# Kernel optimization log

Hardware: AMD Instinct MI355X
Metric: run time of the kernel (lower is better)

## Reference

```python
import jax, jax.numpy as jnp
import numpy as np
import math

B, L, D, H = 2, 2048, 1024, 16
HS = D // H  # head size 64


def setup_inputs() -> dict:
    key = jax.random.key(0)
    ks = jax.random.split(key, 4)
    s = 1.0 / math.sqrt(D)
    return {
        "x": jax.random.normal(ks[0], (B, L, D), dtype=jnp.float32),
        "mask": jnp.zeros((B, 1, L, L), dtype=jnp.float32),
        "Wq": jax.random.normal(ks[1], (D, D), dtype=jnp.float32) * s,
        "bq": jnp.zeros((D,), dtype=jnp.float32),
        "Wk": jax.random.normal(ks[2], (D, D), dtype=jnp.float32) * s,
        "bk": jnp.zeros((D,), dtype=jnp.float32),
        "Wv": jax.random.normal(ks[3], (D, D), dtype=jnp.float32) * s,
        "bv": jnp.zeros((D,), dtype=jnp.float32),
    }


def reference(x, mask, Wq, bq, Wk, bk, Wv, bv):
    # projections: torch Linear is x @ W.T + b
    q = (x @ Wq.T + bq).reshape(B, L, H, HS).transpose(0, 2, 1, 3)  # [B,H,L,hs]
    k = (x @ Wk.T + bk).reshape(B, L, H, HS).transpose(0, 2, 1, 3)
    v = (x @ Wv.T + bv).reshape(B, L, H, HS).transpose(0, 2, 1, 3)
    scores = jnp.einsum("bhqd,bhkd->bhqk", q, k) / math.sqrt(HS) + mask
    attn = jax.nn.softmax(scores, axis=-1)  # dropout p=0.0 -> identity
    out = jnp.einsum("bhqk,bhkd->bhqd", attn, v)
    return out.transpose(0, 2, 1, 3).reshape(B, L, D)
```

## Files before the change

kernel.cpp:

```cpp
#include <hip/hip_runtime.h>
#include <cstdint>

#define SEQ 2048
#define DMODEL 1024
#define NHEAD 16
#define HEADSZ 64

typedef __attribute__((ext_vector_type(4))) float f32x4;
typedef __attribute__((ext_vector_type(8))) short short8;
typedef __attribute__((ext_vector_type(4))) unsigned short u16x4;

#define AS1 __attribute__((address_space(1)))
#define AS3 __attribute__((address_space(3)))

__device__ __forceinline__ void gload_lds16(const void* g, void* l) {
  __builtin_amdgcn_global_load_lds((const AS1 void*)g, (AS3 void*)l, 16, 0, 0);
}

__device__ __forceinline__ unsigned short f2bf(float f) {
  unsigned u = __float_as_uint(f);
  u += 0x7fffu + ((u >> 16) & 1u);
  return (unsigned short)(u >> 16);
}

__global__ __launch_bounds__(256) void convert_kernel(
    const float* __restrict__ x, const float* __restrict__ wq,
    const float* __restrict__ wk, const float* __restrict__ wv,
    unsigned short* __restrict__ xb, unsigned short* __restrict__ wb) {
  const long i = ((long)blockIdx.x * 256 + threadIdx.x) * 4;
  const float* src;
  unsigned short* dst;
  if (i < (1L << 22)) {
    src = x + i; dst = xb + i;
  } else {
    const long j = i - (1L << 22);
    dst = wb + j;
    if (j < (1L << 20))        src = wq + j;
    else if (j < (2L << 20))   src = wk + (j - (1L << 20));
    else                       src = wv + (j - (2L << 20));
  }
  f32x4 v = *(const f32x4*)src;
  u16x4 o;
  o.x = f2bf(v.x); o.y = f2bf(v.y); o.z = f2bf(v.z); o.w = f2bf(v.w);
  *(u16x4*)dst = o;
}

__global__ __launch_bounds__(256) void qkv_gemm(
    const unsigned short* __restrict__ xb, const unsigned short* __restrict__ wb,
    const float* __restrict__ bq, const float* __restrict__ bk,
    const float* __restrict__ bv,
    unsigned short* __restrict__ qo, unsigned short* __restrict__ ko,
    unsigned short* __restrict__ vto) {
  __shared__ __attribute__((aligned(16))) unsigned short Sh[2][128 * 64];
  unsigned short* As = &Sh[0][0];
  unsigned short* Bs = &Sh[1][0];

  const int bid = blockIdx.x;
  const int swz = (bid & 7) * 96 + (bid >> 3);
  const int tm = swz / 24, tn = swz % 24;
  const int m0 = tm * 128, n0 = tn * 128;
  const int tsel = n0 >> 10;
  const int t = threadIdx.x;
  const int lane = t & 63, wid = t >> 6;
  const int wr = wid >> 1, wc = wid & 1;
  const int r16 = lane & 15, g4 = lane >> 4;

  f32x4 acc[4][4] = {};

  const unsigned short* ga0 = xb + (long)(m0 + (t >> 3)) * 1024 + (t & 7) * 8;
  const unsigned short* gb0 = wb + (long)(n0 + (t >> 3)) * 1024 + (t & 7) * 8;
  char* lA = (char*)As + wid * 1024;
  char* lB = (char*)Bs + wid * 1024;

  for (int ks = 0; ks < 16; ++ks) {
    const unsigned short* ga = ga0 + ks * 64;
    const unsigned short* gb = gb0 + ks * 64;
#pragma unroll
    for (int r = 0; r < 4; ++r) {
      gload_lds16(ga + r * 32 * 1024, lA + r * 4096);
      gload_lds16(gb + r * 32 * 1024, lB + r * 4096);
    }
    __syncthreads();
#pragma unroll
    for (int kk = 0; kk < 2; ++kk) {
      short8 af[4], bf[4];
#pragma unroll
      for (int mi = 0; mi < 4; ++mi)
        af[mi] = *(const short8*)((const char*)As +
                 (wr * 64 + mi * 16 + r16) * 128 + kk * 64 + g4 * 16);
#pragma unroll
      for (int ni = 0; ni < 4; ++ni)
        bf[ni] = *(const short8*)((const char*)Bs +
                 (wc * 64 + ni * 16 + r16) * 128 + kk * 64 + g4 * 16);
      if (tsel < 2) {
#pragma unroll
        for (int mi = 0; mi < 4; ++mi)
#pragma unroll
          for (int ni = 0; ni < 4; ++ni)
            acc[mi][ni] = __builtin_amdgcn_mfma_f32_16x16x32_bf16(
                bf[ni], af[mi], acc[mi][ni], 0, 0, 0);
      } else {
#pragma unroll
        for (int mi = 0; mi < 4; ++mi)
#pragma unroll
          for (int ni = 0; ni < 4; ++ni)
            acc[mi][ni] = __builtin_amdgcn_mfma_f32_16x16x32_bf16(
                af[mi], bf[ni], acc[mi][ni], 0, 0, 0);
      }
    }
    __syncthreads();
  }

  const int bb = m0 >> 11;
  const int lbase = m0 & 2047;
  const int h0n = n0 & 1023;
  unsigned short* T = As;

  if (tsel < 2) {
    const float* bias = tsel == 0 ? bq : bk;
    unsigned short* dst01 = tsel == 0 ? qo : ko;
#pragma unroll
    for (int ni = 0; ni < 4; ++ni) {
      const int nlb = wc * 64 + ni * 16 + g4 * 4;
      const f32x4 b4 = *(const f32x4*)(bias + h0n + nlb);
#pragma unroll
      for (int mi = 0; mi < 4; ++mi) {
        const int ml = wr * 64 + mi * 16 + r16;
        u16x4 pk;
#pragma unroll
        for (int i = 0; i < 4; ++i) pk[i] = f2bf(acc[mi][ni][i] + b4[i]);
        int byteoff = ml * 256 + nlb * 2;
        byteoff ^= (ml & 7) << 4;
        *(u16x4*)((char*)T + byteoff) = pk;
      }
    }
    __syncthreads();
#pragma unroll
    for (int p = 0; p < 8; ++p) {
      const int ml = p * 16 + (t >> 4);
      int byteoff = ml * 256 + ((t & 15) << 4);
      byteoff ^= (ml & 7) << 4;
      short8 row = *(const short8*)((const char*)T + byteoff);
      const int nd = h0n + (t & 15) * 8;
      const int h = nd >> 6, hs = nd & 63;
      *(short8*)(dst01 + ((long)(bb * NHEAD + h) * SEQ + lbase + ml) * 64 + hs) = row;
    }
  } else {
#pragma unroll
    for (int ni = 0; ni < 4; ++ni) {
      const int nl = wc * 64 + ni * 16 + r16;
      const float bval = bv[h0n + nl];
#pragma unroll
      for (int mi = 0; mi < 4; ++mi) {
        const int mlb = wr * 64 + mi * 16 + g4 * 4;
        u16x4 pk;
#pragma unroll
        for (int i = 0; i < 4; ++i) pk[i] = f2bf(acc[mi][ni][i] + bval);
        int byteoff = nl * 256 + mlb * 2;
        byteoff ^= (nl & 7) << 4;
        *(u16x4*)((char*)T + byteoff) = pk;
      }
    }
    __syncthreads();
#pragma unroll
    for (int p = 0; p < 8; ++p) {
      const int nl = p * 16 + (t >> 4);
      int byteoff = nl * 256 + ((t & 15) << 4);
      byteoff ^= (nl & 7) << 4;
      short8 row = *(const short8*)((const char*)T + byteoff);
      const int nd = h0n + nl;
      const int h = nd >> 6, hs = nd & 63;
      *(short8*)(vto + ((((long)(bb * NHEAD + h)) << 6) + hs) * SEQ + lbase +
                 (t & 15) * 8) = row;
    }
  }
}

__global__ __launch_bounds__(256, 4) void attn_kernel(
    const unsigned short* __restrict__ qb, const unsigned short* __restrict__ kb,
    const unsigned short* __restrict__ vtb, const float* __restrict__ mask,
    float* __restrict__ out) {
  __shared__ __attribute__((aligned(16))) unsigned short Qs[64 * 64];
  __shared__ __attribute__((aligned(16))) unsigned short Ks[2][64 * 64];
  __shared__ __attribute__((aligned(16))) unsigned short Vs[2][64 * 64];

  const int bid = blockIdx.x;
  const int swz = (bid & 7) * 128 + (bid >> 3);
  const int h = swz & 15, rest = swz >> 4;
  const int qt = rest & 31, b = rest >> 5;
  const int bh = b * NHEAD + h;

  const unsigned short* qg = qb + (long)bh * SEQ * 64 + qt * 64 * 64;
  const unsigned short* kg = kb + (long)bh * SEQ * 64;
  const unsigned short* vg = vtb + (long)bh * 64 * SEQ;
  const float* mg = mask + (long)b * SEQ * SEQ + (long)(qt * 64) * SEQ;

  const int t = threadIdx.x;
  const int lane = t & 63, w = t >> 6;
  const int r16 = lane & 15, g4 = lane >> 4;
  const int rowa = t >> 3;
  const int csel = ((t & 7) ^ (rowa & 7)) * 8;
  const int swzr = (r16 & 7);

  auto stageKV = [&](int ktile, int buf) {
#pragma unroll
    for (int r = 0; r < 2; ++r) {
      gload_lds16(kg + (long)(ktile * 64 + r * 32 + rowa) * 64 + csel,
                  (char*)Ks + buf * 8192 + r * 4096 + w * 1024);
      gload_lds16(vg + (long)(r * 32 + rowa) * SEQ + ktile * 64 + csel,
                  (char*)Vs + buf * 8192 + r * 4096 + w * 1024);
    }
  };

#pragma unroll
  for (int r = 0; r < 2; ++r)
    gload_lds16(qg + (r * 256 + t) * 8, (char*)Qs + r * 4096 + w * 1024);
  stageKV(0, 0);
  __syncthreads();

  short8 qf[2];
#pragma unroll
  for (int kk = 0; kk < 2; ++kk)
    qf[kk] = *(const short8*)((const char*)Qs +
              (w * 16 + r16) * 128 + kk * 64 + g4 * 16);
  char* Pw = (char*)Qs + w * 2048;

  float m_st[4], l_st[4];
  f32x4 o_acc[4] = {};
#pragma unroll
  for (int i = 0; i < 4; ++i) { m_st[i] = -1e30f; l_st[i] = 0.f; }

  int cur = 0;
  for (int kt = 0; kt < 32; ++kt) {
    if (kt < 31) stageKV(kt + 1, cur ^ 1);

    const char* Kb = (const char*)Ks + cur * 8192;
    const char* Vb = (const char*)Vs + cur * 8192;

    float mv[4][4];
#pragma unroll
    for (int nf = 0; nf < 4; ++nf)
#pragma unroll
      for (int i = 0; i < 4; ++i)
        mv[nf][i] = mg[(long)(w * 16 + g4 * 4 + i) * SEQ +
                       kt * 64 + nf * 16 + r16];

    f32x4 s[4];
#pragma unroll
    for (int nf = 0; nf < 4; ++nf) {
      f32x4 z = {};
#pragma unroll
      for (int kk = 0; kk < 2; ++kk) {
        short8 kf = *(const short8*)(Kb + (nf * 16 + r16) * 128 +
                     (((kk * 4 + g4) ^ swzr) << 4));
        z = __builtin_amdgcn_mfma_f32_16x16x32_bf16(qf[kk], kf, z, 0, 0, 0);
      }
      s[nf] = z;
    }
#pragma unroll
    for (int nf = 0; nf < 4; ++nf)
#pragma unroll
      for (int i = 0; i < 4; ++i)
        s[nf][i] = s[nf][i] * 0.125f + mv[nf][i];

    float pm[4];
#pragma unroll
    for (int i = 0; i < 4; ++i)
      pm[i] = fmaxf(fmaxf(s[0][i], s[1][i]), fmaxf(s[2][i], s[3][i]));
#pragma unroll
    for (int x = 1; x <= 8; x <<= 1)
#pragma unroll
      for (int i = 0; i < 4; ++i)
        pm[i] = fmaxf(pm[i], __shfl_xor(pm[i], x, 64));
    float alpha[4], rs[4];
#pragma unroll
    for (int i = 0; i < 4; ++i) {
      const float mn = fmaxf(m_st[i], pm[i]);
      alpha[i] = __expf(m_st[i] - mn);
      m_st[i] = mn;
      rs[i] = 0.f;
    }
#pragma unroll
    for (int nf = 0; nf < 4; ++nf)
#pragma unroll
      for (int i = 0; i < 4; ++i) {
        const float p = __expf(s[nf][i] - m_st[i]);
        rs[i] += p;
        const int q = g4 * 4 + i;
        int byteoff = q * 128 + (nf * 16 + r16) * 2;
        byteoff ^= (q & 7) << 4;
        *(unsigned short*)(Pw + byteoff) = f2bf(p);
      }
#pragma unroll
    for (int x = 1; x <= 8; x <<= 1)
#pragma unroll
      for (int i = 0; i < 4; ++i)
        rs[i] += __shfl_xor(rs[i], x, 64);
#pragma unroll
    for (int i = 0; i < 4; ++i)
      l_st[i] = l_st[i] * alpha[i] + rs[i];
#pragma unroll
    for (int nd = 0; nd < 4; ++nd)
#pragma unroll
      for (int i = 0; i < 4; ++i)
        o_acc[nd][i] *= alpha[i];

    asm volatile("s_waitcnt lgkmcnt(0)" ::: "memory");
    short8 pa[2];
#pragma unroll
    for (int kk = 0; kk < 2; ++kk)
      pa[kk] = *(const short8*)(Pw + r16 * 128 + (((kk * 4 + g4) ^ swzr) << 4));
#pragma unroll
    for (int nd = 0; nd < 4; ++nd) {
      f32x4 z = o_acc[nd];
#pragma unroll
      for (int kk = 0; kk < 2; ++kk) {
        short8 vf = *(const short8*)(Vb + (nd * 16 + r16) * 128 +
                     (((kk * 4 + g4) ^ swzr) << 4));
        z = __builtin_amdgcn_mfma_f32_16x16x32_bf16(pa[kk], vf, z, 0, 0, 0);
      }
      o_acc[nd] = z;
    }

    __syncthreads();
    cur ^= 1;
  }

  float* ob = out + (long)b * SEQ * DMODEL + (long)(qt * 64) * DMODEL + h * 64;
#pragma unroll
  for (int nd = 0; nd < 4; ++nd)
#pragma unroll
    for (int i = 0; i < 4; ++i) {
      const int qrow = w * 16 + g4 * 4 + i;
      ob[(long)qrow * DMODEL + nd * 16 + r16] = o_acc[nd][i] / l_st[i];
    }
}

extern "C" void kernel_launch(void* const* d_in, const int* in_sizes, int n_in,
                              void* d_out, int out_size, void* d_ws, size_t ws_size,
                              hipStream_t stream) {
  const float* x    = (const float*)d_in[0];
  const float* mask = (const float*)d_in[1];
  const float* Wq   = (const float*)d_in[2];
  const float* bq   = (const float*)d_in[3];
  const float* Wk   = (const float*)d_in[4];
  const float* bk   = (const float*)d_in[5];
  const float* Wv   = (const float*)d_in[6];
  const float* bv   = (const float*)d_in[7];
  float* out = (float*)d_out;

  char* ws = (char*)d_ws;
  unsigned short* xb  = (unsigned short*)(ws);
  unsigned short* wb  = (unsigned short*)(ws + (8L << 20));
  unsigned short* qo  = (unsigned short*)(ws + (14L << 20));
  unsigned short* ko  = (unsigned short*)(ws + (22L << 20));
  unsigned short* vto = (unsigned short*)(ws + (30L << 20));

  convert_kernel<<<7168, 256, 0, stream>>>(x, Wq, Wk, Wv, xb, wb);
  qkv_gemm<<<768, 256, 0, stream>>>(xb, wb, bq, bk, bv, qo, ko, vto);
  attn_kernel<<<1024, 256, 0, stream>>>(qo, ko, vto, mask, out);
}
```

Before: 268.3 us.

## Restructure attention to 32x32 MFMA with 128-row query tiles and register P

```diff
diff --git a/kernel.cpp b/kernel.cpp
--- a/kernel.cpp
+++ b/kernel.cpp
@@ -7,8 +7,10 @@
 #define HEADSZ 64
 
 typedef __attribute__((ext_vector_type(4))) float f32x4;
+typedef __attribute__((ext_vector_type(16))) float f32x16;
 typedef __attribute__((ext_vector_type(8))) short short8;
 typedef __attribute__((ext_vector_type(4))) unsigned short u16x4;
+typedef __attribute__((ext_vector_type(4))) unsigned int u32x4;
 
 #define AS1 __attribute__((address_space(1)))
 #define AS3 __attribute__((address_space(3)))
@@ -21,6 +23,10 @@
   unsigned u = __float_as_uint(f);
   u += 0x7fffu + ((u >> 16) & 1u);
   return (unsigned short)(u >> 16);
+}
+
+__device__ __forceinline__ unsigned pack2bf(float lo, float hi) {
+  return (unsigned)f2bf(lo) | ((unsigned)f2bf(hi) << 16);
 }
 
 __global__ __launch_bounds__(256) void convert_kernel(
@@ -176,59 +182,54 @@
   }
 }
 
-__global__ __launch_bounds__(256, 4) void attn_kernel(
+__global__ __launch_bounds__(256, 2) void attn_kernel(
     const unsigned short* __restrict__ qb, const unsigned short* __restrict__ kb,
     const unsigned short* __restrict__ vtb, const float* __restrict__ mask,
     float* __restrict__ out) {
-  __shared__ __attribute__((aligned(16))) unsigned short Qs[64 * 64];
-  __shared__ __attribute__((aligned(16))) unsigned short Ks[2][64 * 64];
-  __shared__ __attribute__((aligned(16))) unsigned short Vs[2][64 * 64];
+  __shared__ __attribute__((aligned(16))) char lds[34816];
+  unsigned short* Ks = (unsigned short*)lds;
+  unsigned short* Vs = (unsigned short*)(lds + 16384);
 
   const int bid = blockIdx.x;
-  const int swz = (bid & 7) * 128 + (bid >> 3);
-  const int h = swz & 15, rest = swz >> 4;
-  const int qt = rest & 31, b = rest >> 5;
+  const int swz = (bid & 7) * 64 + (bid >> 3);
+  const int h = swz & 15, grp = swz >> 4;
+  const int qt = grp & 15, b = grp >> 4;
   const int bh = b * NHEAD + h;
 
-  const unsigned short* qg = qb + (long)bh * SEQ * 64 + qt * 64 * 64;
+  const int t = threadIdx.x;
+  const int lane = t & 63, w = t >> 6;
+  const int lq = lane & 31;
+  const int hi = lane >> 5;
+
+  const unsigned short* qg = qb + (long)bh * SEQ * 64;
   const unsigned short* kg = kb + (long)bh * SEQ * 64;
   const unsigned short* vg = vtb + (long)bh * 64 * SEQ;
-  const float* mg = mask + (long)b * SEQ * SEQ + (long)(qt * 64) * SEQ;
-
-  const int t = threadIdx.x;
-  const int lane = t & 63, w = t >> 6;
-  const int r16 = lane & 15, g4 = lane >> 4;
-  const int rowa = t >> 3;
-  const int csel = ((t & 7) ^ (rowa & 7)) * 8;
-  const int swzr = (r16 & 7);
-
-  auto stageKV = [&](int ktile, int buf) {
+  const int q0 = qt * 128 + w * 32;
+  const float* mrow = mask + (long)b * SEQ * SEQ + (long)(q0 + lq) * SEQ;
+
+  auto stageKV = [&](int kt, int buf) {
 #pragma unroll
     for (int r = 0; r < 2; ++r) {
-      gload_lds16(kg + (long)(ktile * 64 + r * 32 + rowa) * 64 + csel,
-                  (char*)Ks + buf * 8192 + r * 4096 + w * 1024);
-      gload_lds16(vg + (long)(r * 32 + rowa) * SEQ + ktile * 64 + csel,
-                  (char*)Vs + buf * 8192 + r * 4096 + w * 1024);
+      const int row = w * 16 + r * 8 + (lane >> 3);
+      const int gsw = ((lane & 7) ^ (row & 7)) * 8;
+      gload_lds16(kg + (long)(kt * 64 + row) * 64 + gsw,
+                  (char*)Ks + buf * 8192 + w * 2048 + r * 1024);
+      gload_lds16(vg + (long)row * SEQ + kt * 64 + gsw,
+                  (char*)Vs + buf * 8192 + w * 2048 + r * 1024);
     }
   };
 
-#pragma unroll
-  for (int r = 0; r < 2; ++r)
-    gload_lds16(qg + (r * 256 + t) * 8, (char*)Qs + r * 4096 + w * 1024);
   stageKV(0, 0);
+
+  short8 qf[4];
+#pragma unroll
+  for (int kk = 0; kk < 4; ++kk)
+    qf[kk] = *(const short8*)(qg + (long)(q0 + lq) * 64 + hi * 8 + kk * 16);
+
+  f32x16 oa0 = {}, oa1 = {};
+  float m_st = -1e30f, l_st = 0.f;
+
   __syncthreads();
-
-  short8 qf[2];
-#pragma unroll
-  for (int kk = 0; kk < 2; ++kk)
-    qf[kk] = *(const short8*)((const char*)Qs +
-              (w * 16 + r16) * 128 + kk * 64 + g4 * 16);
-  char* Pw = (char*)Qs + w * 2048;
-
-  float m_st[4], l_st[4];
-  f32x4 o_acc[4] = {};
-#pragma unroll
-  for (int i = 0; i < 4; ++i) { m_st[i] = -1e30f; l_st[i] = 0.f; }
 
   int cur = 0;
   for (int kt = 0; kt < 32; ++kt) {
@@ -237,103 +238,101 @@
     const char* Kb = (const char*)Ks + cur * 8192;
     const char* Vb = (const char*)Vs + cur * 8192;
 
-    float mv[4][4];
-#pragma unroll
-    for (int nf = 0; nf < 4; ++nf)
-#pragma unroll
-      for (int i = 0; i < 4; ++i)
-        mv[nf][i] = mg[(long)(w * 16 + g4 * 4 + i) * SEQ +
-                       kt * 64 + nf * 16 + r16];
-
-    f32x4 s[4];
-#pragma unroll
-    for (int nf = 0; nf < 4; ++nf) {
-      f32x4 z = {};
-#pragma unroll
-      for (int kk = 0; kk < 2; ++kk) {
-        short8 kf = *(const short8*)(Kb + (nf * 16 + r16) * 128 +
-                     (((kk * 4 + g4) ^ swzr) << 4));
-        z = __builtin_amdgcn_mfma_f32_16x16x32_bf16(qf[kk], kf, z, 0, 0, 0);
-      }
-      s[nf] = z;
-    }
-#pragma unroll
-    for (int nf = 0; nf < 4; ++nf)
-#pragma unroll
-      for (int i = 0; i < 4; ++i)
-        s[nf][i] = s[nf][i] * 0.125f + mv[nf][i];
-
-    float pm[4];
-#pragma unroll
-    for (int i = 0; i < 4; ++i)
-      pm[i] = fmaxf(fmaxf(s[0][i], s[1][i]), fmaxf(s[2][i], s[3][i]));
-#pragma unroll
-    for (int x = 1; x <= 8; x <<= 1)
-#pragma unroll
-      for (int i = 0; i < 4; ++i)
-        pm[i] = fmaxf(pm[i], __shfl_xor(pm[i], x, 64));
-    float alpha[4], rs[4];
-#pragma unroll
-    for (int i = 0; i < 4; ++i) {
-      const float mn = fmaxf(m_st[i], pm[i]);
-      alpha[i] = __expf(m_st[i] - mn);
-      m_st[i] = mn;
-      rs[i] = 0.f;
-    }
-#pragma unroll
-    for (int nf = 0; nf < 4; ++nf)
-#pragma unroll
-      for (int i = 0; i < 4; ++i) {
-        const float p = __expf(s[nf][i] - m_st[i]);
-        rs[i] += p;
-        const int q = g4 * 4 + i;
-        int byteoff = q * 128 + (nf * 16 + r16) * 2;
-        byteoff ^= (q & 7) << 4;
-        *(unsigned short*)(Pw + byteoff) = f2bf(p);
-      }
-#pragma unroll
-    for (int x = 1; x <= 8; x <<= 1)
-#pragma unroll
-      for (int i = 0; i < 4; ++i)
-        rs[i] += __shfl_xor(rs[i], x, 64);
-#pragma unroll
-    for (int i = 0; i < 4; ++i)
-      l_st[i] = l_st[i] * alpha[i] + rs[i];
-#pragma unroll
-    for (int nd = 0; nd < 4; ++nd)
-#pragma unroll
-      for (int i = 0; i < 4; ++i)
-        o_acc[nd][i] *= alpha[i];
-
-    asm volatile("s_waitcnt lgkmcnt(0)" ::: "memory");
-    short8 pa[2];
-#pragma unroll
-    for (int kk = 0; kk < 2; ++kk)
-      pa[kk] = *(const short8*)(Pw + r16 * 128 + (((kk * 4 + g4) ^ swzr) << 4));
-#pragma unroll
-    for (int nd = 0; nd < 4; ++nd) {
-      f32x4 z = o_acc[nd];
-#pragma unroll
-      for (int kk = 0; kk < 2; ++kk) {
-        short8 vf = *(const short8*)(Vb + (nd * 16 + r16) * 128 +
-                     (((kk * 4 + g4) ^ swzr) << 4));
-        z = __builtin_amdgcn_mfma_f32_16x16x32_bf16(pa[kk], vf, z, 0, 0, 0);
-      }
-      o_acc[nd] = z;
+    f32x4 mv[2][4];
+#pragma unroll
+    for (int k2 = 0; k2 < 2; ++k2)
+#pragma unroll
+      for (int g = 0; g < 4; ++g)
+        mv[k2][g] = *(const f32x4*)(mrow + kt * 64 + k2 * 32 + g * 8 + hi * 4);
+
+    f32x16 sa0 = {}, sa1 = {};
+#pragma unroll
+    for (int kk = 0; kk < 4; ++kk) {
+      const int r0 = lq;
+      short8 kf0 = *(const short8*)(Kb + r0 * 128 + (((hi + 2 * kk) ^ (r0 & 7)) << 4));
+      sa0 = __builtin_amdgcn_mfma_f32_32x32x16_bf16(kf0, qf[kk], sa0, 0, 0, 0);
+      const int r1 = 32 + lq;
+      short8 kf1 = *(const short8*)(Kb + r1 * 128 + (((hi + 2 * kk) ^ (r1 & 7)) << 4));
+      sa1 = __builtin_amdgcn_mfma_f32_32x32x16_bf16(kf1, qf[kk], sa1, 0, 0, 0);
+    }
+
+    float s[32];
+#pragma unroll
+    for (int r = 0; r < 16; ++r)
+      s[r] = sa0[r] * 0.125f + mv[0][r >> 2][r & 3];
+#pragma unroll
+    for (int r = 0; r < 16; ++r)
+      s[16 + r] = sa1[r] * 0.125f + mv[1][r >> 2][r & 3];
+
+    float pm = s[0];
+#pragma unroll
+    for (int r = 1; r < 32; ++r) pm = fmaxf(pm, s[r]);
+    pm = fmaxf(pm, __shfl_xor(pm, 32, 64));
+    const float mn = fmaxf(m_st, pm);
+    const float alpha = __expf(m_st - mn);
+    m_st = mn;
+
+    float rs = 0.f;
+#pragma unroll
+    for (int r = 0; r < 32; ++r) { s[r] = __expf(s[r] - mn); rs += s[r]; }
+    rs += __shfl_xor(rs, 32, 64);
+    l_st = l_st * alpha + rs;
+#pragma unroll
+    for (int r = 0; r < 16; ++r) { oa0[r] *= alpha; oa1[r] *= alpha; }
+
+    u32x4 pw[4];
+#pragma unroll
+    for (int kk = 0; kk < 4; ++kk) {
+      const int base = kk * 8;
+      const unsigned X  = pack2bf(s[base + 0], s[base + 1]);
+      const unsigned X2 = pack2bf(s[base + 2], s[base + 3]);
+      const unsigned Y  = pack2bf(s[base + 4], s[base + 5]);
+      const unsigned Y2 = pack2bf(s[base + 6], s[base + 7]);
+      const unsigned Xp  = __shfl_xor(X, 32, 64);
+      const unsigned X2p = __shfl_xor(X2, 32, 64);
+      const unsigned Yp  = __shfl_xor(Y, 32, 64);
+      const unsigned Y2p = __shfl_xor(Y2, 32, 64);
+      pw[kk][0] = hi ? Yp : X;
+      pw[kk][1] = hi ? Y2p : X2;
+      pw[kk][2] = hi ? Y : Xp;
+      pw[kk][3] = hi ? Y2 : X2p;
+    }
+
+#pragma unroll
+    for (int kk = 0; kk < 4; ++kk) {
+      const short8 pf = __builtin_bit_cast(short8, pw[kk]);
+      const int r0 = lq;
+      short8 vf0 = *(const short8*)(Vb + r0 * 128 + (((hi + 2 * kk) ^ (r0 & 7)) << 4));
+      oa0 = __builtin_amdgcn_mfma_f32_32x32x16_bf16(vf0, pf, oa0, 0, 0, 0);
+      const int r1 = 32 + lq;
+      short8 vf1 = *(const short8*)(Vb + r1 * 128 + (((hi + 2 * kk) ^ (r1 & 7)) << 4));
+      oa1 = __builtin_amdgcn_mfma_f32_32x32x16_bf16(vf1, pf, oa1, 0, 0, 0);
     }
 
     __syncthreads();
     cur ^= 1;
   }
 
-  float* ob = out + (long)b * SEQ * DMODEL + (long)(qt * 64) * DMODEL + h * 64;
-#pragma unroll
-  for (int nd = 0; nd < 4; ++nd)
-#pragma unroll
-    for (int i = 0; i < 4; ++i) {
-      const int qrow = w * 16 + g4 * 4 + i;
-      ob[(long)qrow * DMODEL + nd * 16 + r16] = o_acc[nd][i] / l_st[i];
-    }
+  __syncthreads();
+  float* ot = (float*)lds + w * (32 * 68);
+  const float inv_l = 1.f / l_st;
+#pragma unroll
+  for (int g = 0; g < 4; ++g) {
+    f32x4 v0, v1;
+#pragma unroll
+    for (int j = 0; j < 4; ++j) { v0[j] = oa0[g * 4 + j] * inv_l;
+                                  v1[j] = oa1[g * 4 + j] * inv_l; }
+    *(f32x4*)(ot + lq * 68 + g * 8 + hi * 4) = v0;
+    *(f32x4*)(ot + lq * 68 + 32 + g * 8 + hi * 4) = v1;
+  }
+  asm volatile("s_waitcnt lgkmcnt(0)" ::: "memory");
+  float* ob = out + (long)b * SEQ * DMODEL + (long)q0 * DMODEL + h * 64;
+#pragma unroll
+  for (int j = 0; j < 8; ++j) {
+    const int qr = j * 4 + (lane >> 4);
+    f32x4 v4 = *(const f32x4*)(ot + qr * 68 + (lane & 15) * 4);
+    *(f32x4*)(ob + (long)qr * DMODEL + (lane & 15) * 4) = v4;
+  }
 }
 
 extern "C" void kernel_launch(void* const* d_in, const int* in_sizes, int n_in,
@@ -358,5 +357,5 @@
 
   convert_kernel<<<7168, 256, 0, stream>>>(x, Wq, Wk, Wv, xb, wb);
   qkv_gemm<<<768, 256, 0, stream>>>(xb, wb, bq, bk, bv, qo, ko, vto);
-  attn_kernel<<<1024, 256, 0, stream>>>(qo, ko, vto, mask, out);
-}
+  attn_kernel<<<512, 256, 0, stream>>>(qo, ko, vto, mask, out);
+}
```

After: 270.1 us. Within noise of the previous version (+0.6%).
